# Performance work log

Hardware: AMD Instinct MI355X
Metric: run time of the kernel (lower is better)

## Reference

```python
import jax, jax.numpy as jnp
import numpy as np

WINDOW_SIZE = 64  # matches module init

def setup_inputs() -> dict:
    key = jax.random.key(0)
    kq, kk, kv = jax.random.split(key, 3)
    B, S, H, D = 1, 2048, 8, 64
    return {
        "query": jax.random.normal(kq, (B, S, H, D), dtype=jnp.float32),
        "key": jax.random.normal(kk, (B, S, H, D), dtype=jnp.float32),
        "value": jax.random.normal(kv, (B, S, H, D), dtype=jnp.float32),
    }

def reference(query, key, value):
    # Sliding-window (sparse) attention, window [i-w, i+w] inclusive.
    B, S, H, D = query.shape
    w = WINDOW_SIZE
    scale = 1.0 / jnp.sqrt(jnp.float32(D))
    offs = jnp.arange(-w, w + 1)                      # [W], W = 2w+1
    idx = jnp.arange(S)[:, None] + offs[None, :]      # [S, W]
    valid = (idx >= 0) & (idx < S)                    # [S, W]
    idx_c = jnp.clip(idx, 0, S - 1)
    k_win = key[:, idx_c]                             # [B, S, W, H, D]
    v_win = value[:, idx_c]                           # [B, S, W, H, D]
    scores = jnp.einsum('bshd,bswhd->bshw', query * scale, k_win)
    scores = jnp.where(valid[None, :, None, :], scores, -jnp.inf)
    attn = jax.nn.softmax(scores, axis=-1)            # [B, S, H, W]
    out = jnp.einsum('bshw,bswhd->bshd', attn, v_win)
    return out
```

## Files before the change

kernel.cpp:

```cpp
#include <hip/hip_runtime.h>
#include <stdint.h>

#define S_LEN 2048
#define NH    8
#define TQ    32
#define PVT   168
#define PP    168

typedef __attribute__((ext_vector_type(8))) short  short8;
typedef __attribute__((ext_vector_type(4))) float  floatx4;
typedef __attribute__((ext_vector_type(2))) unsigned int uint32x2;

__device__ __forceinline__ uint16_t f2b(float f) {
  uint32_t u = __float_as_uint(f);
  u += 0x7FFFu + ((u >> 16) & 1u);
  return (uint16_t)(u >> 16);
}
__device__ __forceinline__ short8 pack8(float4 a, float4 b) {
  short8 r;
  r[0] = (short)f2b(a.x); r[1] = (short)f2b(a.y);
  r[2] = (short)f2b(a.z); r[3] = (short)f2b(a.w);
  r[4] = (short)f2b(b.x); r[5] = (short)f2b(b.y);
  r[6] = (short)f2b(b.z); r[7] = (short)f2b(b.w);
  return r;
}

__global__ __launch_bounds__(256, 2)
void swa_mfma(const float* __restrict__ Q, const float* __restrict__ K,
              const float* __restrict__ V, float* __restrict__ O) {
  __shared__ __align__(16) uint16_t Vt[64 * PVT];
  __shared__ __align__(16) uint16_t Pw[TQ * PP];
  __shared__ __align__(16) float    Pp[2][16][4];

  const int tile = blockIdx.x;
  const int h    = blockIdx.y;
  const int tid  = threadIdx.x;
  const int g0   = tile * TQ - 64;

#pragma unroll
  for (int it = 0; it < 10; ++it) {
    int task = tid + it * 256;
    int d    = task & 63;
    int cq   = task >> 6;
    int gb   = g0 + (cq << 2);
    float v[4];
#pragma unroll
    for (int k = 0; k < 4; ++k) {
      int g = gb + k;
      g = g < 0 ? 0 : (g > S_LEN - 1 ? S_LEN - 1 : g);
      v[k] = V[((g * NH + h) << 6) + d];
    }
    uint32_t p01 = (uint32_t)f2b(v[0]) | ((uint32_t)f2b(v[1]) << 16);
    uint32_t p23 = (uint32_t)f2b(v[2]) | ((uint32_t)f2b(v[3]) << 16);
    uint32_t* dst = (uint32_t*)&Vt[d * PVT + (cq << 2)];
    dst[0] = p01; dst[1] = p23;
  }

  const int lane = tid & 63;
  const int w    = tid >> 6;
  const int r16  = lane & 15;
  const int quad = lane >> 4;
  const int qt   = w & 1;
  const int half = w >> 1;
  const int NT   = half ? 4 : 6;
  const int kt0  = half ? 6 : 0;

  const int qrow = tile * TQ + qt * 16 + r16;
  const float* qb = Q + ((qrow * NH + h) << 6) + (quad << 3);
  float4 q0 = *(const float4*)(qb);
  float4 q1 = *(const float4*)(qb + 4);
  float4 q2 = *(const float4*)(qb + 32);
  float4 q3 = *(const float4*)(qb + 36);
  const float sc = 0.125f;
  q0.x*=sc;q0.y*=sc;q0.z*=sc;q0.w*=sc;  q1.x*=sc;q1.y*=sc;q1.z*=sc;q1.w*=sc;
  q2.x*=sc;q2.y*=sc;q2.z*=sc;q2.w*=sc;  q3.x*=sc;q3.y*=sc;q3.z*=sc;q3.w*=sc;
  short8 bq0 = pack8(q0, q1);
  short8 bq1 = pack8(q2, q3);

  floatx4 acc[6];
#pragma unroll
  for (int u = 0; u < 6; ++u) acc[u] = (floatx4){0.f, 0.f, 0.f, 0.f};

#pragma unroll
  for (int u = 0; u < 6; ++u) if (u < NT) {
    int g = g0 + (kt0 + u) * 16 + r16;
    g = g < 0 ? 0 : (g > S_LEN - 1 ? S_LEN - 1 : g);
    const float* kb = K + ((g * NH + h) << 6) + (quad << 3);
    float4 k0 = *(const float4*)(kb);
    float4 k1 = *(const float4*)(kb + 4);
    float4 k2 = *(const float4*)(kb + 32);
    float4 k3 = *(const float4*)(kb + 36);
    short8 ak0 = pack8(k0, k1);
    short8 ak1 = pack8(k2, k3);
    acc[u] = __builtin_amdgcn_mfma_f32_16x16x32_bf16(ak0, bq0, acc[u], 0, 0, 0);
    acc[u] = __builtin_amdgcn_mfma_f32_16x16x32_bf16(ak1, bq1, acc[u], 0, 0, 0);
  }

  float mx = -INFINITY;
#pragma unroll
  for (int u = 0; u < 6; ++u) if (u < NT) {
#pragma unroll
    for (int r = 0; r < 4; ++r) {
      int kpos = (kt0 + u) * 16 + (quad << 2) + r;
      int g    = g0 + kpos;
      bool ok  = (g >= 0) && (g < S_LEN) && (g >= qrow - 64) && (g <= qrow + 64);
      float s  = ok ? acc[u][r] : -INFINITY;
      acc[u][r] = s;
      mx = fmaxf(mx, s);
    }
  }
  mx = fmaxf(mx, __shfl_xor(mx, 16, 64));
  mx = fmaxf(mx, __shfl_xor(mx, 32, 64));
  mx = fmaxf(mx, -3.0e38f);

  float sum = 0.f;
  uint32_t* prow = (uint32_t*)&Pw[(qt * 16 + r16) * PP];
#pragma unroll
  for (int u = 0; u < 6; ++u) if (u < NT) {
    float e0 = __expf(acc[u][0] - mx);
    float e1 = __expf(acc[u][1] - mx);
    float e2 = __expf(acc[u][2] - mx);
    float e3 = __expf(acc[u][3] - mx);
    sum += (e0 + e1) + (e2 + e3);
    uint32x2 pw;
    pw[0] = (uint32_t)f2b(e0) | ((uint32_t)f2b(e1) << 16);
    pw[1] = (uint32_t)f2b(e2) | ((uint32_t)f2b(e3) << 16);
    int ci = (kt0 + u) * 16 + (quad << 2);
    *(uint32x2*)&prow[ci >> 1] = pw;
  }
  sum += __shfl_xor(sum, 16, 64);
  sum += __shfl_xor(sum, 32, 64);
  if (quad == 0) {
    Pp[qt][r16][half * 2]     = mx;
    Pp[qt][r16][half * 2 + 1] = sum;
  }

  __syncthreads();

  short8 pa[5];
  const uint16_t* Pr = &Pw[(qt * 16 + r16) * PP + (quad << 3)];
#pragma unroll
  for (int kt = 0; kt < 5; ++kt)
    pa[kt] = *(const short8*)(Pr + kt * 32);

  float ca[4], cb[4];
#pragma unroll
  for (int r = 0; r < 4; ++r) {
    float4 p = *(const float4*)(&Pp[qt][(quad << 2) + r][0]);
    float m  = fmaxf(p.x, p.z);
    float f0 = __expf(p.x - m);
    float f1 = __expf(p.z - m);
    float rs = 1.0f / (f0 * p.y + f1 * p.w);
    ca[r] = f0 * rs;
    cb[r] = f1 * rs;
  }

#pragma unroll
  for (int t = 0; t < 2; ++t) {
    int dt = half * 2 + t;
    const uint16_t* Vr = &Vt[(dt * 16 + r16) * PVT + (quad << 3)];
    floatx4 oA = {0.f, 0.f, 0.f, 0.f};
    floatx4 oB = {0.f, 0.f, 0.f, 0.f};
#pragma unroll
    for (int kt = 0; kt < 3; ++kt)
      oA = __builtin_amdgcn_mfma_f32_16x16x32_bf16(pa[kt], *(const short8*)(Vr + kt * 32), oA, 0, 0, 0);
#pragma unroll
    for (int kt = 3; kt < 5; ++kt)
      oB = __builtin_amdgcn_mfma_f32_16x16x32_bf16(pa[kt], *(const short8*)(Vr + kt * 32), oB, 0, 0, 0);
    int orow = tile * TQ + qt * 16 + (quad << 2);
    int d    = dt * 16 + r16;
#pragma unroll
    for (int r = 0; r < 4; ++r)
      O[(((orow + r) * NH + h) << 6) + d] = ca[r] * oA[r] + cb[r] * oB[r];
  }
}

extern "C" void kernel_launch(void* const* d_in, const int* in_sizes, int n_in,
                              void* d_out, int out_size, void* d_ws, size_t ws_size,
                              hipStream_t stream) {
  const float* Q = (const float*)d_in[0];
  const float* K = (const float*)d_in[1];
  const float* V = (const float*)d_in[2];
  float* O = (float*)d_out;
  dim3 grid(S_LEN / TQ, NH);
  swa_mfma<<<grid, 256, 0, stream>>>(Q, K, V, O);
}
```

Baseline: 75.54 us.

## Split key tiles across four wave groups with 512-thread blocks

Doubles the block to 512 threads, so each 32-query tile is handled by 8 waves instead of 4. Key tiles are split into four groups (4/2/2/2 tiles), and each group computes its own partial softmax max and sum. Four partials are then merged per row, and each wave computes one 16-wide output column slice in the PV step. The aim is shorter per-wave dependency chains and more waves in flight to hide load latency, at the cost of an extra merge and more threads competing for LDS and registers.

```diff
diff --git a/kernel.cpp b/kernel.cpp
--- a/kernel.cpp
+++ b/kernel.cpp
@@ -25,12 +25,12 @@
   return r;
 }
 
-__global__ __launch_bounds__(256, 2)
+__global__ __launch_bounds__(512, 4)
 void swa_mfma(const float* __restrict__ Q, const float* __restrict__ K,
               const float* __restrict__ V, float* __restrict__ O) {
   __shared__ __align__(16) uint16_t Vt[64 * PVT];
   __shared__ __align__(16) uint16_t Pw[TQ * PP];
-  __shared__ __align__(16) float    Pp[2][16][4];
+  __shared__ __align__(16) float    Pp[2][16][8];
 
   const int tile = blockIdx.x;
   const int h    = blockIdx.y;
@@ -38,8 +38,8 @@
   const int g0   = tile * TQ - 64;
 
 #pragma unroll
-  for (int it = 0; it < 10; ++it) {
-    int task = tid + it * 256;
+  for (int it = 0; it < 5; ++it) {
+    int task = tid + it * 512;
     int d    = task & 63;
     int cq   = task >> 6;
     int gb   = g0 + (cq << 2);
@@ -61,9 +61,9 @@
   const int r16  = lane & 15;
   const int quad = lane >> 4;
   const int qt   = w & 1;
-  const int half = w >> 1;
-  const int NT   = half ? 4 : 6;
-  const int kt0  = half ? 6 : 0;
+  const int kq   = w >> 1;
+  const int NT   = (kq == 0) ? 4 : 2;
+  const int kt0  = (kq == 0) ? 0 : 2 + 2 * kq;
 
   const int qrow = tile * TQ + qt * 16 + r16;
   const float* qb = Q + ((qrow * NH + h) << 6) + (quad << 3);
@@ -77,12 +77,12 @@
   short8 bq0 = pack8(q0, q1);
   short8 bq1 = pack8(q2, q3);
 
-  floatx4 acc[6];
+  floatx4 acc[4];
 #pragma unroll
-  for (int u = 0; u < 6; ++u) acc[u] = (floatx4){0.f, 0.f, 0.f, 0.f};
+  for (int u = 0; u < 4; ++u) acc[u] = (floatx4){0.f, 0.f, 0.f, 0.f};
 
 #pragma unroll
-  for (int u = 0; u < 6; ++u) if (u < NT) {
+  for (int u = 0; u < 4; ++u) if (u < NT) {
     int g = g0 + (kt0 + u) * 16 + r16;
     g = g < 0 ? 0 : (g > S_LEN - 1 ? S_LEN - 1 : g);
     const float* kb = K + ((g * NH + h) << 6) + (quad << 3);
@@ -98,14 +98,14 @@
 
   float mx = -INFINITY;
 #pragma unroll
-  for (int u = 0; u < 6; ++u) if (u < NT) {
+  for (int u = 0; u < 4; ++u) if (u < NT) {
 #pragma unroll
-    for (int r = 0; r < 4; ++r) {
-      int kpos = (kt0 + u) * 16 + (quad << 2) + r;
+    for (int rg = 0; rg < 4; ++rg) {
+      int kpos = (kt0 + u) * 16 + (quad << 2) + rg;
       int g    = g0 + kpos;
       bool ok  = (g >= 0) && (g < S_LEN) && (g >= qrow - 64) && (g <= qrow + 64);
-      float s  = ok ? acc[u][r] : -INFINITY;
-      acc[u][r] = s;
+      float s  = ok ? acc[u][rg] : -INFINITY;
+      acc[u][rg] = s;
       mx = fmaxf(mx, s);
     }
   }
@@ -116,7 +116,7 @@
   float sum = 0.f;
   uint32_t* prow = (uint32_t*)&Pw[(qt * 16 + r16) * PP];
 #pragma unroll
-  for (int u = 0; u < 6; ++u) if (u < NT) {
+  for (int u = 0; u < 4; ++u) if (u < NT) {
     float e0 = __expf(acc[u][0] - mx);
     float e1 = __expf(acc[u][1] - mx);
     float e2 = __expf(acc[u][2] - mx);
@@ -131,8 +131,8 @@
   sum += __shfl_xor(sum, 16, 64);
   sum += __shfl_xor(sum, 32, 64);
   if (quad == 0) {
-    Pp[qt][r16][half * 2]     = mx;
-    Pp[qt][r16][half * 2 + 1] = sum;
+    Pp[qt][r16][kq * 2]     = mx;
+    Pp[qt][r16][kq * 2 + 1] = sum;
   }
 
   __syncthreads();
@@ -140,39 +140,42 @@
   short8 pa[5];
   const uint16_t* Pr = &Pw[(qt * 16 + r16) * PP + (quad << 3)];
 #pragma unroll
-  for (int kt = 0; kt < 5; ++kt)
-    pa[kt] = *(const short8*)(Pr + kt * 32);
+  for (int ks = 0; ks < 5; ++ks)
+    pa[ks] = *(const short8*)(Pr + ks * 32);
 
-  float ca[4], cb[4];
+  const int dq = kq;
+  const uint16_t* Vr = &Vt[(dq * 16 + r16) * PVT + (quad << 3)];
+  floatx4 o0 = {0.f,0.f,0.f,0.f};
+  floatx4 o1 = {0.f,0.f,0.f,0.f};
+  floatx4 o2 = {0.f,0.f,0.f,0.f};
+  floatx4 o3 = {0.f,0.f,0.f,0.f};
+  o0 = __builtin_amdgcn_mfma_f32_16x16x32_bf16(pa[0], *(const short8*)(Vr +   0), o0, 0, 0, 0);
+  o0 = __builtin_amdgcn_mfma_f32_16x16x32_bf16(pa[1], *(const short8*)(Vr +  32), o0, 0, 0, 0);
+  o1 = __builtin_amdgcn_mfma_f32_16x16x32_bf16(pa[2], *(const short8*)(Vr +  64), o1, 0, 0, 0);
+  o2 = __builtin_amdgcn_mfma_f32_16x16x32_bf16(pa[3], *(const short8*)(Vr +  96), o2, 0, 0, 0);
+  o3 = __builtin_amdgcn_mfma_f32_16x16x32_bf16(pa[4], *(const short8*)(Vr + 128), o3, 0, 0, 0);
+
+  float c0[4], c1[4], c2[4], c3[4];
 #pragma unroll
-  for (int r = 0; r < 4; ++r) {
-    float4 p = *(const float4*)(&Pp[qt][(quad << 2) + r][0]);
-    float m  = fmaxf(p.x, p.z);
-    float f0 = __expf(p.x - m);
-    float f1 = __expf(p.z - m);
-    float rs = 1.0f / (f0 * p.y + f1 * p.w);
-    ca[r] = f0 * rs;
-    cb[r] = f1 * rs;
+  for (int rg = 0; rg < 4; ++rg) {
+    const float* pp = &Pp[qt][(quad << 2) + rg][0];
+    float4 pA = *(const float4*)(pp);
+    float4 pB = *(const float4*)(pp + 4);
+    float m  = fmaxf(fmaxf(pA.x, pA.z), fmaxf(pB.x, pB.z));
+    float f0 = __expf(pA.x - m);
+    float f1 = __expf(pA.z - m);
+    float f2 = __expf(pB.x - m);
+    float f3 = __expf(pB.z - m);
+    float rs = 1.0f / (f0 * pA.y + f1 * pA.w + f2 * pB.y + f3 * pB.w);
+    c0[rg] = f0 * rs; c1[rg] = f1 * rs; c2[rg] = f2 * rs; c3[rg] = f3 * rs;
   }
 
+  const int orow = tile * TQ + qt * 16 + (quad << 2);
+  const int d    = dq * 16 + r16;
 #pragma unroll
-  for (int t = 0; t < 2; ++t) {
-    int dt = half * 2 + t;
-    const uint16_t* Vr = &Vt[(dt * 16 + r16) * PVT + (quad << 3)];
-    floatx4 oA = {0.f, 0.f, 0.f, 0.f};
-    floatx4 oB = {0.f, 0.f, 0.f, 0.f};
-#pragma unroll
-    for (int kt = 0; kt < 3; ++kt)
-      oA = __builtin_amdgcn_mfma_f32_16x16x32_bf16(pa[kt], *(const short8*)(Vr + kt * 32), oA, 0, 0, 0);
-#pragma unroll
-    for (int kt = 3; kt < 5; ++kt)
-      oB = __builtin_amdgcn_mfma_f32_16x16x32_bf16(pa[kt], *(const short8*)(Vr + kt * 32), oB, 0, 0, 0);
-    int orow = tile * TQ + qt * 16 + (quad << 2);
-    int d    = dt * 16 + r16;
-#pragma unroll
-    for (int r = 0; r < 4; ++r)
-      O[(((orow + r) * NH + h) << 6) + d] = ca[r] * oA[r] + cb[r] * oB[r];
-  }
+  for (int rg = 0; rg < 4; ++rg)
+    O[(((orow + rg) * NH + h) << 6) + d] =
+        c0[rg] * o0[rg] + c1[rg] * o1[rg] + c2[rg] * o2[rg] + c3[rg] * o3[rg];
 }
 
 extern "C" void kernel_launch(void* const* d_in, const int* in_sizes, int n_in,
@@ -183,5 +186,5 @@
   const float* V = (const float*)d_in[2];
   float* O = (float*)d_out;
   dim3 grid(S_LEN / TQ, NH);
-  swa_mfma<<<grid, 256, 0, stream>>>(Q, K, V, O);
+  swa_mfma<<<grid, 512, 0, stream>>>(Q, K, V, O);
 }
```

Measured after the change: 75.37 us. About the same (-0.2%).
